# Optimization experiments

Measured on AMD Instinct MI355X. Metric: run time of the kernel, lower is better.

The kernel has to match this reference:

```python
import jax, jax.numpy as jnp
import numpy as np

N_USER = 8192
N_PRODUCT = 8192
E = 128
D = 64
K = 32
M = 4


def _make_nbrs(m, n, k, n_other, salt):
    # distinct neighbor indices per (metapath, node): step = n_other // k guarantees
    # the k offsets are distinct modulo n_other (matches set-like ragged lists)
    i = np.arange(m)[:, None, None]
    j = np.arange(n)[None, :, None]
    t = np.arange(k)[None, None, :]
    idx = (j * 7 + i * 131 + salt * 17 + t * (n_other // k)) % n_other
    return jnp.asarray(idx, dtype=jnp.int32)


def setup_inputs() -> dict:
    key = jax.random.key(0)
    ks = jax.random.split(key, 16)
    s = 0.1
    return {
        "user": jax.random.normal(ks[0], (N_USER, E), jnp.float32),
        "product": jax.random.normal(ks[1], (N_PRODUCT, E), jnp.float32),
        "V": jax.random.normal(ks[2], (2, M, E, D), jnp.float32) * s,
        "X": jax.random.normal(ks[3], (2, M, 1, D), jnp.float32) * s,
        "W_p": jax.random.normal(ks[4], (2, M, E, D), jnp.float32) * s,
        "B_p": jax.random.normal(ks[5], (2, M, D), jnp.float32) * s,
        "W_q": jax.random.normal(ks[6], (2, M, E, D), jnp.float32) * s,
        "B_q": jax.random.normal(ks[7], (2, M, D), jnp.float32) * s,
        "Q": jax.random.normal(ks[8], (2, M, 1, D), jnp.float32) * s,
        "user_nbrs": _make_nbrs(M, N_USER, K, N_PRODUCT, 0),
        "product_nbrs": _make_nbrs(M, N_PRODUCT, K, N_USER, 1),
    }


def _phase(src, other, nbrs, v, x, w, b, wq, bq, q):
    # src: [n,E], other: [n_other,E], nbrs: [M,n,K] indices into other
    m, n, k = nbrs.shape
    n_other = other.shape[0]
    nbr_emb = other[nbrs]  # [M,n,K,E] ragged gather
    proj_src = jnp.einsum('ne,med->mnd', src, v)          # [M,n,D]
    proj_nbr = jnp.einsum('mnke,med->mnkd', nbr_emb, w)   # [M,n,K,D]
    h = jnp.tanh(proj_src[:, :, None, :] + proj_nbr + b[:, None, None, :])
    scores = jnp.einsum('mnkd,md->mnk', h, x[:, 0])       # [M,n,K]
    # Faithful to torch: non-neighbor logit is -1e-9 for metapath 0; for
    # metapath i>=1 the repeated whole-tensor softmax makes it 1/n_other.
    baseline = jnp.where(jnp.arange(m) == 0,
                         jnp.float32(-1e-9),
                         jnp.float32(1.0) / n_other)      # [M]
    mx = jnp.maximum(scores.max(-1), baseline[:, None])   # [M,n]
    e = jnp.exp(scores - mx[..., None])
    denom = e.sum(-1) + (n_other - k) * jnp.exp(baseline[:, None] - mx)
    A = e / denom[..., None]                              # softmax over full axis
    # H aggregation uses detached attention weights (A.data in torch)
    H = src[None] + jnp.einsum('mnk,mnke->mne', jax.lax.stop_gradient(A), nbr_emb)
    sem = jnp.tanh(jnp.einsum('mne,med->mnd', H, wq) + bq[:, None, :])
    beta_raw = jax.lax.stop_gradient(
        jnp.einsum('mnd,md->mn', sem, q[:, 0]).mean(-1))  # [M], detached (.data)
    beta = jax.nn.softmax(beta_raw)
    return jnp.einsum('m,mne->ne', beta, H)


def reference(user, product, V, X, W_p, B_p, W_q, B_q, Q, user_nbrs, product_nbrs):
    user_out = _phase(user, product, user_nbrs,
                      V[0], X[0], W_p[0], B_p[0], W_q[0], B_q[0], Q[0])
    # product phase attends over the UPDATED user embeddings
    product_out = _phase(product, user_out, product_nbrs,
                         V[1], X[1], W_p[1], B_p[1], W_q[1], B_q[1], Q[1])
    return (user_out, product_out)
```

## Files before the change

kernel.cpp:

```cpp
#include <hip/hip_runtime.h>
#include <hip/hip_bf16.h>

#define NN 8192
#define ED 128
#define DD 64
#define KK 32
#define MM 4

typedef __attribute__((ext_vector_type(8))) short short8;
typedef __attribute__((ext_vector_type(4))) float f32x4;
typedef __attribute__((ext_vector_type(2))) float f32x2;

#if __has_builtin(__builtin_amdgcn_exp2f)
#define EXP2R(x) __builtin_amdgcn_exp2f(x)
#else
#define EXP2R(x) __expf((x) * 0.6931471805599453f)
#endif
#define C2LOG2E 2.8853900817779268f

#if __has_builtin(__builtin_elementwise_fma)
#define FMA2(a, b, c) __builtin_elementwise_fma((a), (b), (c))
#else
__device__ __forceinline__ f32x2 FMA2(f32x2 a, f32x2 b, f32x2 c)
{
    f32x2 r;
    r.x = fmaf(a.x, b.x, c.x);
    r.y = fmaf(a.y, b.y, c.y);
    return r;
}
#endif

__device__ __forceinline__ float ftanh_pre(float v)
{
    return fmaf(-2.0f, __builtin_amdgcn_rcpf(EXP2R(v) + 1.0f), 1.0f);
}
__device__ __forceinline__ float ftanh(float x)
{
    return ftanh_pre(x * C2LOG2E);
}

__device__ __forceinline__ unsigned short f2bf(float x)
{
    __hip_bfloat16 b = __float2bfloat16(x);
    return *reinterpret_cast<unsigned short*>(&b);
}
__device__ __forceinline__ float bflo(unsigned int u) { return __uint_as_float(u << 16); }
__device__ __forceinline__ float bfhi(unsigned int u) { return __uint_as_float(u & 0xFFFF0000u); }
__device__ __forceinline__ float readlane_f(float v, int lane)
{
    return __uint_as_float(__builtin_amdgcn_readlane(__float_as_uint(v), lane));
}

template <int CTRL>
__device__ __forceinline__ float dpp_mov_f(float x)
{
    return __int_as_float(__builtin_amdgcn_update_dpp(
        0, __float_as_int(x), CTRL, 0xF, 0xF, true));
}
template <int CTRL>
__device__ __forceinline__ float dpp_add_f(float x)
{
    return x + dpp_mov_f<CTRL>(x);
}

__global__ __launch_bounds__(256) void prep_kernel(
    const float* __restrict__ user, unsigned short* __restrict__ userB,
    const float* __restrict__ product, unsigned short* __restrict__ productB,
    const float* __restrict__ V, unsigned short* __restrict__ VT,
    const float* __restrict__ Wp, unsigned short* __restrict__ PT,
    const float* __restrict__ Wq, unsigned short* __restrict__ QT)
{
    const int y = blockIdx.y;
    if (y < 2) {
        const float* in = y ? product : user;
        unsigned short* out = y ? productB : userB;
        const int i = blockIdx.x * 256 + threadIdx.x;
        const float4 v = ((const float4*)in)[i];
        uint2 o;
        o.x = (unsigned int)f2bf(v.x) | ((unsigned int)f2bf(v.y) << 16);
        o.y = (unsigned int)f2bf(v.z) | ((unsigned int)f2bf(v.w) << 16);
        ((uint2*)out)[i] = o;
    } else {
        if (blockIdx.x >= 256) return;
        const float* in = (y == 2) ? V : (y == 3) ? Wp : Wq;
        unsigned short* out = (y == 2) ? VT : (y == 3) ? PT : QT;
        const int gid = blockIdx.x * 256 + threadIdx.x;
        const int s   = gid >> 13;
        const int rem = gid & 8191;
        const int e   = rem >> 6;
        const int d   = rem & 63;
        out[((size_t)s * DD + d) * ED + e] = f2bf(in[gid]);
    }
}

__global__ __launch_bounds__(256) void proj3_mfma(
    const unsigned short* __restrict__ emb0,
    const unsigned short* __restrict__ Wt0,
    const float* __restrict__ Bias0,
    float* __restrict__ outF0,
    const unsigned short* __restrict__ emb1,
    const unsigned short* __restrict__ Wt1,
    unsigned short* __restrict__ outB1,
    const unsigned short* __restrict__ Wt2,
    const float* __restrict__ Bias2,
    float* __restrict__ outF2)
{
    const int z    = blockIdx.z;
    const int m    = blockIdx.y;
    const int tid  = threadIdx.x;
    const int wave = tid >> 6;
    const int lane = tid & 63;
    const int nrow = lane & 15;
    const int quad = lane >> 4;
    const int r0   = blockIdx.x * 64 + wave * 16;

    const unsigned short* embB = (z == 0) ? emb0 : emb1;
    const unsigned short* WtB  = (z == 0) ? Wt0 : (z == 1) ? Wt1 : Wt2;

    const short8* A8 = (const short8*)(embB + (size_t)(r0 + nrow) * ED);
    const short8* B8 = (const short8*)(WtB + (size_t)m * DD * ED);

    f32x4 acc0 = {0.f, 0.f, 0.f, 0.f};
    f32x4 acc1 = {0.f, 0.f, 0.f, 0.f};
    f32x4 acc2 = {0.f, 0.f, 0.f, 0.f};
    f32x4 acc3 = {0.f, 0.f, 0.f, 0.f};

    #pragma unroll
    for (int kq = 0; kq < 4; ++kq) {
        const short8 a = A8[kq * 4 + quad];
        const short8 b0 = B8[(0 * 16 + nrow) * 16 + kq * 4 + quad];
        const short8 b1 = B8[(1 * 16 + nrow) * 16 + kq * 4 + quad];
        const short8 b2 = B8[(2 * 16 + nrow) * 16 + kq * 4 + quad];
        const short8 b3 = B8[(3 * 16 + nrow) * 16 + kq * 4 + quad];
        acc0 = __builtin_amdgcn_mfma_f32_16x16x32_bf16(a, b0, acc0, 0, 0, 0);
        acc1 = __builtin_amdgcn_mfma_f32_16x16x32_bf16(a, b1, acc1, 0, 0, 0);
        acc2 = __builtin_amdgcn_mfma_f32_16x16x32_bf16(a, b2, acc2, 0, 0, 0);
        acc3 = __builtin_amdgcn_mfma_f32_16x16x32_bf16(a, b3, acc3, 0, 0, 0);
    }

    f32x4 accs[4] = {acc0, acc1, acc2, acc3};
    if (z == 1) {
        #pragma unroll
        for (int t = 0; t < 4; ++t) {
            const int d = t * 16 + nrow;
            #pragma unroll
            for (int reg = 0; reg < 4; ++reg) {
                const int r = r0 + quad * 4 + reg;
                outB1[((size_t)m * NN + r) * DD + d] =
                    f2bf(EXP2R(accs[t][reg] * C2LOG2E));
            }
        }
    } else {
        const float* Bi = (z == 0) ? Bias0 : Bias2;
        float* oF       = (z == 0) ? outF0 : outF2;
        #pragma unroll
        for (int t = 0; t < 4; ++t) {
            const int d = t * 16 + nrow;
            const float bv = Bi[m * DD + d];
            #pragma unroll
            for (int reg = 0; reg < 4; ++reg) {
                const int r = r0 + quad * 4 + reg;
                oF[((size_t)m * NN + r) * DD + d] =
                    EXP2R((accs[t][reg] + bv) * C2LOG2E);
            }
        }
    }
}

__global__ __launch_bounds__(512) void attn_sem_kernel(
    const float* __restrict__ src,
    const unsigned short* __restrict__ otherB,
    const int*   __restrict__ nbrs,
    const float* __restrict__ S,
    const unsigned short* __restrict__ PnB,
    const float* __restrict__ Xv,
    unsigned short* __restrict__ HoutB,
    const unsigned short* __restrict__ WqT,
    const float* __restrict__ Bq,
    const float* __restrict__ Qv,
    float* __restrict__ bp)
{
    __shared__ __align__(16) unsigned int lh[16][68];
    __shared__ float red_sh[4];

    const int m    = blockIdx.y;
    const int tid  = threadIdx.x;
    const int w    = tid >> 6;
    const int lane = tid & 63;
    const int g    = blockIdx.x * 8 + w;
    const int j0   = g * 2;
    const int j1   = g * 2 + 1;

    const int kr = lane >> 3;
    const int d8 = lane & 7;

    const int jj = (lane < 32) ? j0 : j1;
    const int idxreg = nbrs[((size_t)m * NN + jj) * KK + (lane & 31)];

    int sk0[4], sk1[4];
    #pragma unroll
    for (int i = 0; i < 4; ++i) {
        const int k = i * 8 + kr;
        sk0[i] = __shfl(idxreg, k, 64);
        sk1[i] = __shfl(idxreg, 32 + k, 64);
    }
    uint4 P0[4], P1[4];
    #pragma unroll
    for (int i = 0; i < 4; ++i) {
        P0[i] = ((const uint4*)(PnB + ((size_t)m * NN + sk0[i]) * DD))[d8];
        P1[i] = ((const uint4*)(PnB + ((size_t)m * NN + sk1[i]) * DD))[d8];
    }

    unsigned int g0[KK], g1[KK];
    #pragma unroll
    for (int k = 0; k < KK; ++k) {
        const int ja = __builtin_amdgcn_readlane(idxreg, k);
        const int jb = __builtin_amdgcn_readlane(idxreg, 32 + k);
        g0[k] = ((const unsigned int*)(otherB + (size_t)ja * ED))[lane];
        g1[k] = ((const unsigned int*)(otherB + (size_t)jb * ED))[lane];
    }

    f32x2 S0v[4], S1v[4], m2Xv[4];
    float sumX;
    {
        const float4 a0 = *(const float4*)(S + ((size_t)m * NN + j0) * DD + d8 * 8);
        const float4 a1 = *(const float4*)(S + ((size_t)m * NN + j0) * DD + d8 * 8 + 4);
        const float4 b0 = *(const float4*)(S + ((size_t)m * NN + j1) * DD + d8 * 8);
        const float4 b1 = *(const float4*)(S + ((size_t)m * NN + j1) * DD + d8 * 8 + 4);
        const float4 x0 = *(const float4*)(Xv + (size_t)m * DD + d8 * 8);
        const float4 x1 = *(const float4*)(Xv + (size_t)m * DD + d8 * 8 + 4);
        S0v[0] = (f32x2){a0.x, a0.y}; S0v[1] = (f32x2){a0.z, a0.w};
        S0v[2] = (f32x2){a1.x, a1.y}; S0v[3] = (f32x2){a1.z, a1.w};
        S1v[0] = (f32x2){b0.x, b0.y}; S1v[1] = (f32x2){b0.z, b0.w};
        S1v[2] = (f32x2){b1.x, b1.y}; S1v[3] = (f32x2){b1.z, b1.w};
        m2Xv[0] = (f32x2){-2.0f * x0.x, -2.0f * x0.y};
        m2Xv[1] = (f32x2){-2.0f * x0.z, -2.0f * x0.w};
        m2Xv[2] = (f32x2){-2.0f * x1.x, -2.0f * x1.y};
        m2Xv[3] = (f32x2){-2.0f * x1.z, -2.0f * x1.w};
        sumX = ((x0.x + x0.y) + (x0.z + x0.w)) + ((x1.x + x1.y) + (x1.z + x1.w));
    }
    const float2 hs0 = ((const float2*)(src + (size_t)j0 * ED))[lane];
    const float2 hs1 = ((const float2*)(src + (size_t)j1 * ED))[lane];

    const f32x2 ones = {1.0f, 1.0f};
    float ea0[4], ea1[4];
    #pragma unroll
    for (int i = 0; i < 4; ++i) {
        const unsigned int pw0[4] = {P0[i].x, P0[i].y, P0[i].z, P0[i].w};
        const unsigned int pw1[4] = {P1[i].x, P1[i].y, P1[i].z, P1[i].w};
        f32x2 q0v = {sumX, 0.0f};
        f32x2 q1v = {sumX, 0.0f};
        #pragma unroll
        for (int c = 0; c < 4; ++c) {
            const f32x2 p0 = {bflo(pw0[c]), bfhi(pw0[c])};
            const f32x2 p1 = {bflo(pw1[c]), bfhi(pw1[c])};
            const f32x2 t0 = FMA2(p0, S0v[c], ones);
            const f32x2 t1 = FMA2(p1, S1v[c], ones);
            f32x2 r0, r1;
            r0.x = __builtin_amdgcn_rcpf(t0.x);
            r0.y = __builtin_amdgcn_rcpf(t0.y);
            r1.x = __builtin_amdgcn_rcpf(t1.x);
            r1.y = __builtin_amdgcn_rcpf(t1.y);
            q0v = FMA2(m2Xv[c], r0, q0v);
            q1v = FMA2(m2Xv[c], r1, q1v);
        }
        float q0 = q0v.x + q0v.y;
        float q1 = q1v.x + q1v.y;
        q0 = dpp_add_f<0xB1>(q0);   q1 = dpp_add_f<0xB1>(q1);
        q0 = dpp_add_f<0x4E>(q0);   q1 = dpp_add_f<0x4E>(q1);
        q0 = dpp_add_f<0x141>(q0);  q1 = dpp_add_f<0x141>(q1);
        ea0[i] = q0;
        ea1[i] = q1;
    }

    const float baseline = (m == 0) ? -1e-9f : (1.0f / (float)NN);
    float mx0 = ea0[0], mx1 = ea1[0];
    #pragma unroll
    for (int i = 1; i < 4; ++i) { mx0 = fmaxf(mx0, ea0[i]); mx1 = fmaxf(mx1, ea1[i]); }
    mx0 = fmaxf(mx0, dpp_mov_f<0x128>(mx0));
    mx1 = fmaxf(mx1, dpp_mov_f<0x128>(mx1));
    mx0 = fmaxf(mx0, __shfl_xor(mx0, 16, 64));
    mx1 = fmaxf(mx1, __shfl_xor(mx1, 16, 64));
    mx0 = fmaxf(mx0, __shfl_xor(mx0, 32, 64));
    mx1 = fmaxf(mx1, __shfl_xor(mx1, 32, 64));
    mx0 = fmaxf(mx0, baseline);
    mx1 = fmaxf(mx1, baseline);
    float sum0 = 0.0f, sum1 = 0.0f;
    #pragma unroll
    for (int i = 0; i < 4; ++i) {
        ea0[i] = __expf(ea0[i] - mx0); sum0 += ea0[i];
        ea1[i] = __expf(ea1[i] - mx1); sum1 += ea1[i];
    }
    sum0 = dpp_add_f<0x128>(sum0);
    sum1 = dpp_add_f<0x128>(sum1);
    sum0 += __shfl_xor(sum0, 16, 64);  sum1 += __shfl_xor(sum1, 16, 64);
    sum0 += __shfl_xor(sum0, 32, 64);  sum1 += __shfl_xor(sum1, 32, 64);
    const float inv0 =
        __builtin_amdgcn_rcpf(sum0 + (float)(NN - KK) * __expf(baseline - mx0));
    const float inv1 =
        __builtin_amdgcn_rcpf(sum1 + (float)(NN - KK) * __expf(baseline - mx1));
    #pragma unroll
    for (int i = 0; i < 4; ++i) { ea0[i] *= inv0; ea1[i] *= inv1; }

    f32x2 ha = {hs0.x, hs0.y};
    f32x2 hb = {hs1.x, hs1.y};
    #pragma unroll
    for (int k = 0; k < KK; ++k) {
        const float a0 = readlane_f(ea0[k >> 3], (k & 7) * 8);
        const float a1 = readlane_f(ea1[k >> 3], (k & 7) * 8);
        const f32x2 av0 = {a0, a0};
        const f32x2 av1 = {a1, a1};
        const f32x2 e0 = {bflo(g0[k]), bfhi(g0[k])};
        const f32x2 e1 = {bflo(g1[k]), bfhi(g1[k])};
        ha = FMA2(av0, e0, ha);
        hb = FMA2(av1, e1, hb);
    }
    const unsigned int hu0 =
        (unsigned int)f2bf(ha.x) | ((unsigned int)f2bf(ha.y) << 16);
    const unsigned int hu1 =
        (unsigned int)f2bf(hb.x) | ((unsigned int)f2bf(hb.y) << 16);
    ((unsigned int*)(HoutB + ((size_t)m * NN + j0) * ED))[lane] = hu0;
    ((unsigned int*)(HoutB + ((size_t)m * NN + j1) * ED))[lane] = hu1;

    lh[w * 2    ][lane] = hu0;
    lh[w * 2 + 1][lane] = hu1;
    __syncthreads();

    if (w < 4) {
        const int nrow = lane & 15;
        const int quad = lane >> 4;
        const short8* B8 = (const short8*)(WqT + (size_t)m * DD * ED);
        const short8* A8 = (const short8*)&lh[nrow][0];
        f32x4 acc = {0.f, 0.f, 0.f, 0.f};
        #pragma unroll
        for (int kq = 0; kq < 4; ++kq) {
            const short8 a = A8[kq * 4 + quad];
            const short8 b = B8[(w * 16 + nrow) * 16 + kq * 4 + quad];
            acc = __builtin_amdgcn_mfma_f32_16x16x32_bf16(a, b, acc, 0, 0, 0);
        }
        const int d = w * 16 + nrow;
        const float bq = Bq[m * DD + d];
        const float qv = Qv[m * DD + d];
        float part = 0.0f;
        #pragma unroll
        for (int reg = 0; reg < 4; ++reg)
            part = fmaf(ftanh(acc[reg] + bq), qv, part);
        #pragma unroll
        for (int off = 32; off; off >>= 1) part += __shfl_xor(part, off, 64);
        if (lane == 0) red_sh[w] = part;
    }
    __syncthreads();
    if (tid == 0)
        bp[m * 512 + blockIdx.x] =
            (red_sh[0] + red_sh[1]) + (red_sh[2] + red_sh[3]);
}

__global__ __launch_bounds__(256) void combine_proj(
    const unsigned short* __restrict__ HB,
    const float* __restrict__ bp,
    float* __restrict__ outp,
    unsigned short* __restrict__ outB,
    const unsigned short* __restrict__ WtE,
    unsigned short* __restrict__ EPo)
{
    __shared__ float bw_sh[4];
    const int tid = threadIdx.x;
    if (tid < 64) {
        const int m = tid >> 4, t = tid & 15;
        float s = 0.0f;
        #pragma unroll
        for (int i = 0; i < 32; ++i)
            s += bp[m * 512 + t + i * 16];
        s += __shfl_xor(s, 1, 64);
        s += __shfl_xor(s, 2, 64);
        s += __shfl_xor(s, 4, 64);
        s += __shfl_xor(s, 8, 64);
        const float v = s * (1.0f / (float)NN);
        float mx = v;
        mx = fmaxf(mx, __shfl_xor(mx, 16, 64));
        mx = fmaxf(mx, __shfl_xor(mx, 32, 64));
        const float e = expf(v - mx);
        float es = e;
        es += __shfl_xor(es, 16, 64);
        es += __shfl_xor(es, 32, 64);
        if (t == 0) bw_sh[m] = e / es;
    }
    __syncthreads();
    const float bw0 = bw_sh[0], bw1 = bw_sh[1], bw2 = bw_sh[2], bw3 = bw_sh[3];

    const int mB   = blockIdx.y;
    const bool writer = (mB == 0);
    const int wave = tid >> 6;
    const int lane = tid & 63;
    const int nrow = lane & 15;
    const int quad = lane >> 4;
    const int r0   = blockIdx.x * 64 + wave * 16;
    const int r    = r0 + nrow;
    const size_t st = (size_t)NN * ED;

    short8 afrag[4];
    #pragma unroll
    for (int kq = 0; kq < 4; ++kq) {
        const int col = kq * 32 + quad * 8;
        const size_t off = (size_t)r * ED + col;
        const uint4 v0 = *(const uint4*)(HB + 0 * st + off);
        const uint4 v1 = *(const uint4*)(HB + 1 * st + off);
        const uint4 v2 = *(const uint4*)(HB + 2 * st + off);
        const uint4 v3 = *(const uint4*)(HB + 3 * st + off);
        const unsigned int u0[4] = {v0.x, v0.y, v0.z, v0.w};
        const unsigned int u1[4] = {v1.x, v1.y, v1.z, v1.w};
        const unsigned int u2[4] = {v2.x, v2.y, v2.z, v2.w};
        const unsigned int u3[4] = {v3.x, v3.y, v3.z, v3.w};
        float a[8];
        #pragma unroll
        for (int c = 0; c < 4; ++c) {
            a[2*c]   = fmaf(bw0, bflo(u0[c]), fmaf(bw1, bflo(u1[c]),
                       fmaf(bw2, bflo(u2[c]), bw3 * bflo(u3[c]))));
            a[2*c+1] = fmaf(bw0, bfhi(u0[c]), fmaf(bw1, bfhi(u1[c]),
                       fmaf(bw2, bfhi(u2[c]), bw3 * bfhi(u3[c]))));
        }
        uint4 ob;
        ob.x = (unsigned int)f2bf(a[0]) | ((unsigned int)f2bf(a[1]) << 16);
        ob.y = (unsigned int)f2bf(a[2]) | ((unsigned int)f2bf(a[3]) << 16);
        ob.z = (unsigned int)f2bf(a[4]) | ((unsigned int)f2bf(a[5]) << 16);
        ob.w = (unsigned int)f2bf(a[6]) | ((unsigned int)f2bf(a[7]) << 16);
        if (writer) {
            float4 o1; o1.x = a[0]; o1.y = a[1]; o1.z = a[2]; o1.w = a[3];
            float4 o2; o2.x = a[4]; o2.y = a[5]; o2.z = a[6]; o2.w = a[7];
            *(float4*)(outp + off)     = o1;
            *(float4*)(outp + off + 4) = o2;
            *(uint4*)(outB + off) = ob;
        }
        union { uint4 u; short8 s; } pk;
        pk.u = ob;
        afrag[kq] = pk.s;
    }

    const short8* B8 = (const short8*)(WtE + (size_t)mB * DD * ED);
    f32x4 acc0 = {0.f, 0.f, 0.f, 0.f};
    f32x4 acc1 = {0.f, 0.f, 0.f, 0.f};
    f32x4 acc2 = {0.f, 0.f, 0.f, 0.f};
    f32x4 acc3 = {0.f, 0.f, 0.f, 0.f};
    #pragma unroll
    for (int kq = 0; kq < 4; ++kq) {
        const short8 a = afrag[kq];
        const short8 w0 = B8[(0 * 16 + nrow) * 16 + kq * 4 + quad];
        const short8 w1 = B8[(1 * 16 + nrow) * 16 + kq * 4 + quad];
        const short8 w2 = B8[(2 * 16 + nrow) * 16 + kq * 4 + quad];
        const short8 w3 = B8[(3 * 16 + nrow) * 16 + kq * 4 + quad];
        acc0 = __builtin_amdgcn_mfma_f32_16x16x32_bf16(a, w0, acc0, 0, 0, 0);
        acc1 = __builtin_amdgcn_mfma_f32_16x16x32_bf16(a, w1, acc1, 0, 0, 0);
        acc2 = __builtin_amdgcn_mfma_f32_16x16x32_bf16(a, w2, acc2, 0, 0, 0);
        acc3 = __builtin_amdgcn_mfma_f32_16x16x32_bf16(a, w3, acc3, 0, 0, 0);
    }
    f32x4 accs[4] = {acc0, acc1, acc2, acc3};
    #pragma unroll
    for (int t = 0; t < 4; ++t) {
        const int d = t * 16 + nrow;
        #pragma unroll
        for (int reg = 0; reg < 4; ++reg) {
            const int rr = r0 + quad * 4 + reg;
            EPo[((size_t)mB * NN + rr) * DD + d] =
                f2bf(EXP2R(accs[t][reg] * C2LOG2E));
        }
    }
}

__global__ __launch_bounds__(256) void combine_kernel(
    const unsigned short* __restrict__ HB,
    const float* __restrict__ bp,
    float* __restrict__ outp)
{
    __shared__ float bw_sh[4];
    const int tid = threadIdx.x;
    if (tid < 64) {
        const int m = tid >> 4, t = tid & 15;
        float s = 0.0f;
        #pragma unroll
        for (int i = 0; i < 32; ++i)
            s += bp[m * 512 + t + i * 16];
        s += __shfl_xor(s, 1, 64);
        s += __shfl_xor(s, 2, 64);
        s += __shfl_xor(s, 4, 64);
        s += __shfl_xor(s, 8, 64);
        const float v = s * (1.0f / (float)NN);
        float mx = v;
        mx = fmaxf(mx, __shfl_xor(mx, 16, 64));
        mx = fmaxf(mx, __shfl_xor(mx, 32, 64));
        const float e = expf(v - mx);
        float es = e;
        es += __shfl_xor(es, 16, 64);
        es += __shfl_xor(es, 32, 64);
        if (t == 0) bw_sh[m] = e / es;
    }
    __syncthreads();

    const int i = blockIdx.x * 256 + tid;
    const size_t st = (size_t)NN * ED / 4;
    const uint2* h = (const uint2*)HB;
    float r0 = 0.f, r1 = 0.f, r2 = 0.f, r3 = 0.f;
    #pragma unroll
    for (int s = 0; s < MM; ++s) {
        const float b = bw_sh[s];
        const uint2 v = h[s * st + i];
        r0 = fmaf(b, bflo(v.x), r0);
        r1 = fmaf(b, bfhi(v.x), r1);
        r2 = fmaf(b, bflo(v.y), r2);
        r3 = fmaf(b, bfhi(v.y), r3);
    }
    float4 o; o.x = r0; o.y = r1; o.z = r2; o.w = r3;
    ((float4*)outp)[i] = o;
}

extern "C" void kernel_launch(void* const* d_in, const int* in_sizes, int n_in,
                              void* d_out, int out_size, void* d_ws, size_t ws_size,
                              hipStream_t stream)
{
    const float* user    = (const float*)d_in[0];
    const float* product = (const float*)d_in[1];
    const float* V   = (const float*)d_in[2];
    const float* X   = (const float*)d_in[3];
    const float* W_p = (const float*)d_in[4];
    const float* B_p = (const float*)d_in[5];
    const float* W_q = (const float*)d_in[6];
    const float* B_q = (const float*)d_in[7];
    const float* Q   = (const float*)d_in[8];
    const int* user_nbrs    = (const int*)d_in[9];
    const int* product_nbrs = (const int*)d_in[10];

    float* out  = (float*)d_out;
    float* out0 = out;
    float* out1 = out + (size_t)NN * ED;

    float* ws = (float*)d_ws;
    float* bp = ws;
    float* S  = bp + 2048;
    float* S2 = S + (size_t)MM * NN * DD;
    unsigned short* us = (unsigned short*)(S2 + (size_t)MM * NN * DD);
    unsigned short* PnB      = us;
    unsigned short* HB       = PnB + (size_t)MM * NN * DD;
    unsigned short* userB    = HB + (size_t)MM * NN * ED;
    unsigned short* productB = userB + (size_t)NN * ED;
    unsigned short* oB       = productB + (size_t)NN * ED;
    unsigned short* VT       = oB + (size_t)NN * ED;
    unsigned short* PT       = VT + (size_t)2 * MM * DD * ED;
    unsigned short* QT       = PT + (size_t)2 * MM * DD * ED;

    const size_t MED = (size_t)MM * ED * DD;
    const size_t MD  = (size_t)MM * DD;

    const dim3 gP(NN / 64, MM, 3);
    const dim3 gA(NN / 16, MM);
    const dim3 gC(NN / 64, MM);
    const int cBlocks = (NN * ED / 4) / 256;

    prep_kernel<<<dim3(1024, 5), 256, 0, stream>>>(user, userB, product, productB,
                                                   V, VT, W_p, PT, W_q, QT);

    proj3_mfma<<<gP, 256, 0, stream>>>(userB, VT, B_p, S,
                                       productB, PT, PnB,
                                       VT + MED, B_p + MD, S2);

    attn_sem_kernel<<<gA, 512, 0, stream>>>(user, productB, user_nbrs,
                                            S, PnB, X, HB,
                                            QT, B_q, Q, bp);

    combine_proj<<<gC, 256, 0, stream>>>(HB, bp, out0, oB,
                                         PT + MED, PnB);

    attn_sem_kernel<<<gA, 512, 0, stream>>>(product, oB, product_nbrs,
                                            S2, PnB, X + MD, HB,
                                            QT + MED, B_q + MD, Q + MD, bp);

    combine_kernel<<<cBlocks, 256, 0, stream>>>(HB, bp, out1);
}
```

Baseline: 215.7 us.

## Split wave into half-waves per node and stream neighbor gathers with triple buffer

Each wave now handles two nodes by assigning each 32-lane half to one node, instead of every lane working on both nodes. Neighbor rows are loaded as uint2 per lane and streamed through a 3-slot rotating buffer, replacing the 64 preloaded gather registers. Attention weights are broadcast with cross-lane shuffles instead of readlanes. This is meant to cut register pressure and raise occupancy, at the cost of more shuffle (LDS-path) traffic and less memory-level parallelism per wave.

```diff
diff --git a/kernel.cpp b/kernel.cpp
--- a/kernel.cpp
+++ b/kernel.cpp
@@ -46,9 +46,9 @@
 }
 __device__ __forceinline__ float bflo(unsigned int u) { return __uint_as_float(u << 16); }
 __device__ __forceinline__ float bfhi(unsigned int u) { return __uint_as_float(u & 0xFFFF0000u); }
-__device__ __forceinline__ float readlane_f(float v, int lane)
-{
-    return __uint_as_float(__builtin_amdgcn_readlane(__float_as_uint(v), lane));
+__device__ __forceinline__ float shfl_f(float v, int srcLane)
+{
+    return __shfl(v, srcLane, 64);
 }
 
 template <int CTRL>
@@ -187,143 +187,115 @@
     const int tid  = threadIdx.x;
     const int w    = tid >> 6;
     const int lane = tid & 63;
+    const int l5   = lane & 31;
+    const int h    = lane >> 5;
     const int g    = blockIdx.x * 8 + w;
-    const int j0   = g * 2;
-    const int j1   = g * 2 + 1;
-
-    const int kr = lane >> 3;
+    const int j    = g * 2 + h;
+
+    const int kr = l5 >> 3;
     const int d8 = lane & 7;
-
-    const int jj = (lane < 32) ? j0 : j1;
-    const int idxreg = nbrs[((size_t)m * NN + jj) * KK + (lane & 31)];
-
-    int sk0[4], sk1[4];
-    #pragma unroll
-    for (int i = 0; i < 4; ++i) {
-        const int k = i * 8 + kr;
-        sk0[i] = __shfl(idxreg, k, 64);
-        sk1[i] = __shfl(idxreg, 32 + k, 64);
-    }
-    uint4 P0[4], P1[4];
-    #pragma unroll
-    for (int i = 0; i < 4; ++i) {
-        P0[i] = ((const uint4*)(PnB + ((size_t)m * NN + sk0[i]) * DD))[d8];
-        P1[i] = ((const uint4*)(PnB + ((size_t)m * NN + sk1[i]) * DD))[d8];
-    }
-
-    unsigned int g0[KK], g1[KK];
-    #pragma unroll
-    for (int k = 0; k < KK; ++k) {
-        const int ja = __builtin_amdgcn_readlane(idxreg, k);
-        const int jb = __builtin_amdgcn_readlane(idxreg, 32 + k);
-        g0[k] = ((const unsigned int*)(otherB + (size_t)ja * ED))[lane];
-        g1[k] = ((const unsigned int*)(otherB + (size_t)jb * ED))[lane];
-    }
-
-    f32x2 S0v[4], S1v[4], m2Xv[4];
+    const int hbase = lane & 32;
+
+    const int idxreg = nbrs[((size_t)m * NN + j) * KK + l5];
+
+    int sk[8];
+    #pragma unroll
+    for (int i = 0; i < 8; ++i)
+        sk[i] = __shfl(idxreg, hbase + i * 4 + kr, 64);
+    uint4 P[8];
+    #pragma unroll
+    for (int i = 0; i < 8; ++i)
+        P[i] = ((const uint4*)(PnB + ((size_t)m * NN + sk[i]) * DD))[d8];
+
+    uint2 buf[3];
+    {
+        const int jk0 = __shfl(idxreg, hbase + 0, 64);
+        const int jk1 = __shfl(idxreg, hbase + 1, 64);
+        buf[0] = ((const uint2*)(otherB + (size_t)jk0 * ED))[l5];
+        buf[1] = ((const uint2*)(otherB + (size_t)jk1 * ED))[l5];
+    }
+
+    f32x2 Sv[4], m2Xv[4];
     float sumX;
     {
-        const float4 a0 = *(const float4*)(S + ((size_t)m * NN + j0) * DD + d8 * 8);
-        const float4 a1 = *(const float4*)(S + ((size_t)m * NN + j0) * DD + d8 * 8 + 4);
-        const float4 b0 = *(const float4*)(S + ((size_t)m * NN + j1) * DD + d8 * 8);
-        const float4 b1 = *(const float4*)(S + ((size_t)m * NN + j1) * DD + d8 * 8 + 4);
+        const float4 a0 = *(const float4*)(S + ((size_t)m * NN + j) * DD + d8 * 8);
+        const float4 a1 = *(const float4*)(S + ((size_t)m * NN + j) * DD + d8 * 8 + 4);
         const float4 x0 = *(const float4*)(Xv + (size_t)m * DD + d8 * 8);
         const float4 x1 = *(const float4*)(Xv + (size_t)m * DD + d8 * 8 + 4);
-        S0v[0] = (f32x2){a0.x, a0.y}; S0v[1] = (f32x2){a0.z, a0.w};
-        S0v[2] = (f32x2){a1.x, a1.y}; S0v[3] = (f32x2){a1.z, a1.w};
-        S1v[0] = (f32x2){b0.x, b0.y}; S1v[1] = (f32x2){b0.z, b0.w};
-        S1v[2] = (f32x2){b1.x, b1.y}; S1v[3] = (f32x2){b1.z, b1.w};
+        Sv[0] = (f32x2){a0.x, a0.y}; Sv[1] = (f32x2){a0.z, a0.w};
+        Sv[2] = (f32x2){a1.x, a1.y}; Sv[3] = (f32x2){a1.z, a1.w};
         m2Xv[0] = (f32x2){-2.0f * x0.x, -2.0f * x0.y};
         m2Xv[1] = (f32x2){-2.0f * x0.z, -2.0f * x0.w};
         m2Xv[2] = (f32x2){-2.0f * x1.x, -2.0f * x1.y};
         m2Xv[3] = (f32x2){-2.0f * x1.z, -2.0f * x1.w};
         sumX = ((x0.x + x0.y) + (x0.z + x0.w)) + ((x1.x + x1.y) + (x1.z + x1.w));
     }
-    const float2 hs0 = ((const float2*)(src + (size_t)j0 * ED))[lane];
-    const float2 hs1 = ((const float2*)(src + (size_t)j1 * ED))[lane];
+    const float4 hs = ((const float4*)(src + (size_t)j * ED))[l5];
 
     const f32x2 ones = {1.0f, 1.0f};
-    float ea0[4], ea1[4];
-    #pragma unroll
-    for (int i = 0; i < 4; ++i) {
-        const unsigned int pw0[4] = {P0[i].x, P0[i].y, P0[i].z, P0[i].w};
-        const unsigned int pw1[4] = {P1[i].x, P1[i].y, P1[i].z, P1[i].w};
-        f32x2 q0v = {sumX, 0.0f};
-        f32x2 q1v = {sumX, 0.0f};
+    float ea[8];
+    #pragma unroll
+    for (int i = 0; i < 8; ++i) {
+        const unsigned int pw[4] = {P[i].x, P[i].y, P[i].z, P[i].w};
+        f32x2 qv = {sumX, 0.0f};
         #pragma unroll
         for (int c = 0; c < 4; ++c) {
-            const f32x2 p0 = {bflo(pw0[c]), bfhi(pw0[c])};
-            const f32x2 p1 = {bflo(pw1[c]), bfhi(pw1[c])};
-            const f32x2 t0 = FMA2(p0, S0v[c], ones);
-            const f32x2 t1 = FMA2(p1, S1v[c], ones);
-            f32x2 r0, r1;
-            r0.x = __builtin_amdgcn_rcpf(t0.x);
-            r0.y = __builtin_amdgcn_rcpf(t0.y);
-            r1.x = __builtin_amdgcn_rcpf(t1.x);
-            r1.y = __builtin_amdgcn_rcpf(t1.y);
-            q0v = FMA2(m2Xv[c], r0, q0v);
-            q1v = FMA2(m2Xv[c], r1, q1v);
-        }
-        float q0 = q0v.x + q0v.y;
-        float q1 = q1v.x + q1v.y;
-        q0 = dpp_add_f<0xB1>(q0);   q1 = dpp_add_f<0xB1>(q1);
-        q0 = dpp_add_f<0x4E>(q0);   q1 = dpp_add_f<0x4E>(q1);
-        q0 = dpp_add_f<0x141>(q0);  q1 = dpp_add_f<0x141>(q1);
-        ea0[i] = q0;
-        ea1[i] = q1;
+            const f32x2 p = {bflo(pw[c]), bfhi(pw[c])};
+            const f32x2 t = FMA2(p, Sv[c], ones);
+            f32x2 r;
+            r.x = __builtin_amdgcn_rcpf(t.x);
+            r.y = __builtin_amdgcn_rcpf(t.y);
+            qv = FMA2(m2Xv[c], r, qv);
+        }
+        float q = qv.x + qv.y;
+        q = dpp_add_f<0xB1>(q);
+        q = dpp_add_f<0x4E>(q);
+        q = dpp_add_f<0x141>(q);
+        ea[i] = q;
     }
 
     const float baseline = (m == 0) ? -1e-9f : (1.0f / (float)NN);
-    float mx0 = ea0[0], mx1 = ea1[0];
-    #pragma unroll
-    for (int i = 1; i < 4; ++i) { mx0 = fmaxf(mx0, ea0[i]); mx1 = fmaxf(mx1, ea1[i]); }
-    mx0 = fmaxf(mx0, dpp_mov_f<0x128>(mx0));
-    mx1 = fmaxf(mx1, dpp_mov_f<0x128>(mx1));
-    mx0 = fmaxf(mx0, __shfl_xor(mx0, 16, 64));
-    mx1 = fmaxf(mx1, __shfl_xor(mx1, 16, 64));
-    mx0 = fmaxf(mx0, __shfl_xor(mx0, 32, 64));
-    mx1 = fmaxf(mx1, __shfl_xor(mx1, 32, 64));
-    mx0 = fmaxf(mx0, baseline);
-    mx1 = fmaxf(mx1, baseline);
-    float sum0 = 0.0f, sum1 = 0.0f;
-    #pragma unroll
-    for (int i = 0; i < 4; ++i) {
-        ea0[i] = __expf(ea0[i] - mx0); sum0 += ea0[i];
-        ea1[i] = __expf(ea1[i] - mx1); sum1 += ea1[i];
-    }
-    sum0 = dpp_add_f<0x128>(sum0);
-    sum1 = dpp_add_f<0x128>(sum1);
-    sum0 += __shfl_xor(sum0, 16, 64);  sum1 += __shfl_xor(sum1, 16, 64);
-    sum0 += __shfl_xor(sum0, 32, 64);  sum1 += __shfl_xor(sum1, 32, 64);
-    const float inv0 =
-        __builtin_amdgcn_rcpf(sum0 + (float)(NN - KK) * __expf(baseline - mx0));
-    const float inv1 =
-        __builtin_amdgcn_rcpf(sum1 + (float)(NN - KK) * __expf(baseline - mx1));
-    #pragma unroll
-    for (int i = 0; i < 4; ++i) { ea0[i] *= inv0; ea1[i] *= inv1; }
-
-    f32x2 ha = {hs0.x, hs0.y};
-    f32x2 hb = {hs1.x, hs1.y};
+    float mx = ea[0];
+    #pragma unroll
+    for (int i = 1; i < 8; ++i) mx = fmaxf(mx, ea[i]);
+    mx = fmaxf(mx, dpp_mov_f<0x128>(mx));
+    mx = fmaxf(mx, __shfl_xor(mx, 16, 64));
+    mx = fmaxf(mx, baseline);
+    float sum = 0.0f;
+    #pragma unroll
+    for (int i = 0; i < 8; ++i) {
+        ea[i] = __expf(ea[i] - mx);
+        sum += ea[i];
+    }
+    sum = dpp_add_f<0x128>(sum);
+    sum += __shfl_xor(sum, 16, 64);
+    const float inv =
+        __builtin_amdgcn_rcpf(sum + (float)(NN - KK) * __expf(baseline - mx));
+    #pragma unroll
+    for (int i = 0; i < 8; ++i) ea[i] *= inv;
+
+    f32x2 hA = {hs.x, hs.y};
+    f32x2 hB = {hs.z, hs.w};
     #pragma unroll
     for (int k = 0; k < KK; ++k) {
-        const float a0 = readlane_f(ea0[k >> 3], (k & 7) * 8);
-        const float a1 = readlane_f(ea1[k >> 3], (k & 7) * 8);
-        const f32x2 av0 = {a0, a0};
-        const f32x2 av1 = {a1, a1};
-        const f32x2 e0 = {bflo(g0[k]), bfhi(g0[k])};
-        const f32x2 e1 = {bflo(g1[k]), bfhi(g1[k])};
-        ha = FMA2(av0, e0, ha);
-        hb = FMA2(av1, e1, hb);
-    }
-    const unsigned int hu0 =
-        (unsigned int)f2bf(ha.x) | ((unsigned int)f2bf(ha.y) << 16);
-    const unsigned int hu1 =
-        (unsigned int)f2bf(hb.x) | ((unsigned int)f2bf(hb.y) << 16);
-    ((unsigned int*)(HoutB + ((size_t)m * NN + j0) * ED))[lane] = hu0;
-    ((unsigned int*)(HoutB + ((size_t)m * NN + j1) * ED))[lane] = hu1;
-
-    lh[w * 2    ][lane] = hu0;
-    lh[w * 2 + 1][lane] = hu1;
+        const int slot = k % 3;
+        if (k < KK - 2) {
+            const int jk = __shfl(idxreg, hbase + k + 2, 64);
+            buf[(k + 2) % 3] = ((const uint2*)(otherB + (size_t)jk * ED))[l5];
+        }
+        const float a = __shfl(ea[k >> 2], hbase + (k & 3) * 8, 64);
+        const f32x2 av = {a, a};
+        const f32x2 elo = {bflo(buf[slot].x), bfhi(buf[slot].x)};
+        const f32x2 ehi = {bflo(buf[slot].y), bfhi(buf[slot].y)};
+        hA = FMA2(av, elo, hA);
+        hB = FMA2(av, ehi, hB);
+    }
+    uint2 hu;
+    hu.x = (unsigned int)f2bf(hA.x) | ((unsigned int)f2bf(hA.y) << 16);
+    hu.y = (unsigned int)f2bf(hB.x) | ((unsigned int)f2bf(hB.y) << 16);
+    ((uint2*)(HoutB + ((size_t)m * NN + j) * ED))[l5] = hu;
+
+    *(uint2*)&lh[w * 2 + h][l5 * 2] = hu;
     __syncthreads();
 
     if (w < 4) {
```

New measurement: 179.5 us. -16.8%, faster.
